# Performance work log

Hardware: AMD Instinct MI355X
Metric: run time of the kernel (lower is better)

Reference implementation:

```python
import jax, jax.numpy as jnp
import numpy as np

B, S, H = 256, 1, 2048
Q_SIZE = 4096        # num_heads * head_dim = 32 * 128
QKV = 4 * H          # expected_linear_qkv = 8192
K_SZ = 4             # conv kernel size
C = 32               # ssm channels
WSCALE = 0.02


def setup_inputs() -> dict:
    key = jax.random.key(0)
    ks = jax.random.split(key, 13)
    return {
        "hidden_states": jax.random.normal(ks[0], (B, S, H), jnp.float32),
        "W_qkv": jax.random.normal(ks[1], (QKV, H), jnp.float32) * WSCALE,
        "b_qkv": jax.random.normal(ks[2], (QKV,), jnp.float32) * WSCALE,
        "W_gate": jax.random.normal(ks[3], (2 * H, H), jnp.float32) * WSCALE,
        "W_alpha": jax.random.normal(ks[4], (C, H), jnp.float32) * WSCALE,
        "W_beta": jax.random.normal(ks[5], (C, H), jnp.float32) * WSCALE,
        "W_out": jax.random.normal(ks[6], (H, 2 * H), jnp.float32) * WSCALE,
        "ssm_state_a": jax.random.normal(ks[7], (C,), jnp.float32),
        "ssm_dt_bias": jax.random.normal(ks[8], (C,), jnp.float32),
        "ssm_norm_weight": jnp.ones((128,), jnp.float32),
        "conv_kernel": jax.random.normal(ks[9], (QKV, K_SZ), jnp.float32) * WSCALE,
        "ssm_state": jax.random.normal(ks[10], (B, C), jnp.float32),
        "conv_state": jax.random.normal(ks[11], (B, K_SZ, QKV), jnp.float32),
    }


def reference(hidden_states, W_qkv, b_qkv, W_gate, W_alpha, W_beta, W_out,
              ssm_state_a, ssm_dt_bias, ssm_norm_weight, conv_kernel,
              ssm_state, conv_state):
    bsz = hidden_states.shape[0]
    # qkv projection (decode: only last token matters downstream)
    qkv = jnp.einsum('bsh,dh->bsd', hidden_states, W_qkv) + b_qkv  # [B,S,4H]
    mixed_qkv = qkv[:, -1, :].astype(jnp.float32)                  # [B,4H]
    hidden_last = hidden_states[:, -1, :]                          # [B,H]

    # roll conv state and append current token, then causal conv1d step
    cs = jnp.concatenate([conv_state[:, 1:, :], mixed_qkv[:, None, :]], axis=1)  # [B,K,4H]
    conv_out = jnp.einsum('bkd,dk->bd', cs, conv_kernel)           # [B,4H]

    target_size = conv_out.shape[-1] - Q_SIZE                      # 2H = 4096
    k_size = target_size // 2                                      # 2048
    core_base = conv_out[:, Q_SIZE:]                               # [B,2H]
    k_proj = core_base[:, :k_size]
    v_proj = core_base[:, k_size:]

    # alpha/beta gating of the SSM state
    a = hidden_last @ W_alpha.T                                    # [B,C]
    b = hidden_last @ W_beta.T                                     # [B,C]
    g = -jnp.exp(ssm_state_a)[None, :] * jax.nn.softplus(a + ssm_dt_bias[None, :])
    beta = jax.nn.sigmoid(b)

    group_width = k_size // C                                      # 64
    v_group = v_proj[:, :group_width * C].reshape(bsz, C, group_width).mean(-1)
    k_group = k_proj[:, :group_width * C].reshape(bsz, C, group_width).mean(-1)

    new_state = jnp.exp(g) * ssm_state + beta * v_group            # [B,C]
    state_signal = new_state * jax.nn.sigmoid(k_group)             # [B,C]

    repeat_factor = target_size // C                               # 128
    expanded = jnp.repeat(state_signal, repeat_factor, axis=-1)[:, :target_size]

    core = core_base + expanded
    core = core * jax.lax.rsqrt(jnp.mean(core * core, axis=-1, keepdims=True) + 1e-6)
    gate = jax.nn.sigmoid(hidden_last @ W_gate.T).astype(jnp.float32)
    core = core * gate * jnp.mean(ssm_norm_weight)
    core = core.astype(hidden_states.dtype)

    out = (core @ W_out.T)[:, None, :]                             # [B,1,H]
    return out
```

## Files before the change

kernel.cpp:

```cpp
#include <hip/hip_runtime.h>
#include <hip/hip_bf16.h>
#include <stdint.h>

#define BSZ 256
#define HDIM 2048
#define NQ 4096
#define N1 8320
#define K1 2048
#define N3 2048
#define K3 4096

typedef __attribute__((ext_vector_type(8))) short bf16x8;
typedef __attribute__((ext_vector_type(4))) float f32x4;

__device__ __forceinline__ unsigned short f2bf(float f) {
  union { float f; unsigned u; } v; v.f = f;
  unsigned r = v.u + 0x7fffu + ((v.u >> 16) & 1u);
  return (unsigned short)(r >> 16);
}

__device__ __forceinline__ void gload_lds16(const void* g, void* lds_uniform) {
  __builtin_amdgcn_global_load_lds(
      (const __attribute__((address_space(1))) unsigned int*)g,
      (__attribute__((address_space(3))) unsigned int*)lds_uniform, 16, 0, 0);
}

__global__ __launch_bounds__(256) void cvt_kernel(const float* __restrict__ x,
                                                  unsigned short* __restrict__ y) {
  int i = (blockIdx.x * 256 + threadIdx.x) * 8;
  float4 a = *(const float4*)(x + i);
  float4 b = *(const float4*)(x + i + 4);
  ushort4 o0 = { f2bf(a.x), f2bf(a.y), f2bf(a.z), f2bf(a.w) };
  ushort4 o1 = { f2bf(b.x), f2bf(b.y), f2bf(b.z), f2bf(b.w) };
  *(ushort4*)(y + i) = o0;
  *(ushort4*)(y + i + 4) = o1;
}

__global__ __launch_bounds__(256) void gemm1_kernel(
    const unsigned short* __restrict__ A16,
    const float* __restrict__ Wqkv, const float* __restrict__ Wgate,
    const float* __restrict__ Walpha, const float* __restrict__ Wbeta,
    float* __restrict__ P) {
  __shared__ unsigned short sA[128 * 32];
  __shared__ unsigned short sB[128 * 32];
  const int tid = threadIdx.x;
  const int lane = tid & 63, wv = tid >> 6;
  const int wr = wv >> 1, wc = wv & 1;
  const int rt = blockIdx.x * 128;
  const int n0 = blockIdx.y * 128;
  const int kbase = blockIdx.z * 1024;

  f32x4 acc[4][4];
#pragma unroll
  for (int i = 0; i < 4; i++)
#pragma unroll
    for (int j = 0; j < 4; j++) { f32x4 z = {0.f, 0.f, 0.f, 0.f}; acc[i][j] = z; }

  for (int ks = 0; ks < 32; ks++) {
    const int k0 = kbase + ks * 32;
#pragma unroll
    for (int it = 0; it < 2; it++) {
      int chunk = (it * 4 + wv) * 1024;
      int f = chunk + lane * 16;
      const char* g = (const char*)A16 + (size_t)(rt + (f >> 6)) * (K1 * 2) + k0 * 2 + (f & 63);
      gload_lds16(g, (char*)sA + chunk);
    }
#pragma unroll
    for (int it = 0; it < 4; it++) {
      int flat = it * 256 + tid;
      int brow = flat >> 3, c4 = flat & 7;
      int n = n0 + brow;
      const float* src;
      if (n < 4096)       src = Wqkv  + (size_t)(4096 + n) * K1;
      else if (n < 8192)  src = Wgate + (size_t)(n - 4096) * K1;
      else if (n < 8224)  src = Walpha + (size_t)(n - 8192) * K1;
      else if (n < 8256)  src = Wbeta + (size_t)(n - 8224) * K1;
      else                src = Walpha;
      float4 v = *(const float4*)(src + k0 + c4 * 4);
      ushort4 o = { f2bf(v.x), f2bf(v.y), f2bf(v.z), f2bf(v.w) };
      *(ushort4*)(sB + brow * 32 + c4 * 4) = o;
    }
    __syncthreads();
    bf16x8 aF[4], bF[4];
#pragma unroll
    for (int i = 0; i < 4; i++)
      aF[i] = *(const bf16x8*)(sA + (wr * 64 + i * 16 + (lane & 15)) * 32 + (lane >> 4) * 8);
#pragma unroll
    for (int j = 0; j < 4; j++)
      bF[j] = *(const bf16x8*)(sB + (wc * 64 + j * 16 + (lane & 15)) * 32 + (lane >> 4) * 8);
#pragma unroll
    for (int i = 0; i < 4; i++)
#pragma unroll
      for (int j = 0; j < 4; j++)
        acc[i][j] = __builtin_amdgcn_mfma_f32_16x16x32_bf16(aF[i], bF[j], acc[i][j], 0, 0, 0);
    __syncthreads();
  }
  float* Pz = P + (size_t)blockIdx.z * (BSZ * (size_t)N1);
#pragma unroll
  for (int i = 0; i < 4; i++) {
    int row = rt + wr * 64 + i * 16 + (lane >> 4) * 4;
#pragma unroll
    for (int j = 0; j < 4; j++) {
      int col = n0 + wc * 64 + j * 16 + (lane & 15);
#pragma unroll
      for (int r = 0; r < 4; r++)
        Pz[(size_t)(row + r) * N1 + col] = acc[i][j][r];
    }
  }
}

__global__ __launch_bounds__(256) void fuse_kernel(
    const float* __restrict__ P,
    const float* __restrict__ bqkv,
    const float* __restrict__ ck,
    const float* __restrict__ cstate,
    const float* __restrict__ ssa,
    const float* __restrict__ dtb,
    const float* __restrict__ nw,
    const float* __restrict__ sstate,
    unsigned short* __restrict__ C16) {
  __shared__ __align__(16) float cb[4096];
  __shared__ float gsum[64];
  __shared__ float ssl[32];
  __shared__ float red[8];
  __shared__ float mw;
  const int b = blockIdx.x, tid = threadIdx.x;
  const float* P0 = P + (size_t)b * N1;
  const float* P1 = P + (size_t)(BSZ + b) * N1;

  if (tid < 64) gsum[tid] = 0.f;
  if (tid == 0) mw = 0.f;
  __syncthreads();
  if (tid < 128) atomicAdd(&mw, nw[tid]);

#pragma unroll
  for (int it = 0; it < 4; it++) {
    int j = (it * 256 + tid) * 4;
    float4 q0 = *(const float4*)(P0 + j);
    float4 q1 = *(const float4*)(P1 + j);
    float4 bq = *(const float4*)(bqkv + NQ + j);
    float mqx = q0.x + q1.x + bq.x, mqy = q0.y + q1.y + bq.y;
    float mqz = q0.z + q1.z + bq.z, mqw = q0.w + q1.w + bq.w;
    const float* csb = cstate + (size_t)b * 4 * 8192 + NQ + j;
    float4 c1 = *(const float4*)(csb + 1 * 8192);
    float4 c2 = *(const float4*)(csb + 2 * 8192);
    float4 c3 = *(const float4*)(csb + 3 * 8192);
    float4 k0v = *(const float4*)(ck + (size_t)(NQ + j) * 4);
    float4 k1v = *(const float4*)(ck + (size_t)(NQ + j + 1) * 4);
    float4 k2v = *(const float4*)(ck + (size_t)(NQ + j + 2) * 4);
    float4 k3v = *(const float4*)(ck + (size_t)(NQ + j + 3) * 4);
    float4 cbv;
    cbv.x = c1.x * k0v.x + c2.x * k0v.y + c3.x * k0v.z + mqx * k0v.w;
    cbv.y = c1.y * k1v.x + c2.y * k1v.y + c3.y * k1v.z + mqy * k1v.w;
    cbv.z = c1.z * k2v.x + c2.z * k2v.y + c3.z * k2v.z + mqz * k2v.w;
    cbv.w = c1.w * k3v.x + c2.w * k3v.y + c3.w * k3v.z + mqw * k3v.w;
    *(float4*)(cb + j) = cbv;
    float s = cbv.x + cbv.y + cbv.z + cbv.w;
    int g = (j < 2048) ? (j >> 6) : (32 + ((j - 2048) >> 6));
    atomicAdd(&gsum[g], s);
  }
  __syncthreads();

  if (tid < 32) {
    float a  = P0[2 * NQ + tid] + P1[2 * NQ + tid];
    float bc = P0[2 * NQ + 32 + tid] + P1[2 * NQ + 32 + tid];
    float kg = gsum[tid] * (1.f / 64.f);
    float vg = gsum[32 + tid] * (1.f / 64.f);
    float x = a + dtb[tid];
    float sp = fmaxf(x, 0.f) + log1pf(expf(-fabsf(x)));
    float g = -expf(ssa[tid]) * sp;
    float beta = 1.f / (1.f + expf(-bc));
    float ns = expf(g) * sstate[b * 32 + tid] + beta * vg;
    ssl[tid] = ns * (1.f / (1.f + expf(-kg)));
  }
  __syncthreads();

  float sq = 0.f;
  float4 c1r[4];
#pragma unroll
  for (int it = 0; it < 4; it++) {
    int j = (it * 256 + tid) * 4;
    float4 v = *(const float4*)(cb + j);
    float sv = ssl[j >> 7];
    v.x += sv; v.y += sv; v.z += sv; v.w += sv;
    c1r[it] = v;
    sq += v.x * v.x + v.y * v.y + v.z * v.z + v.w * v.w;
  }
#pragma unroll
  for (int off = 32; off > 0; off >>= 1) sq += __shfl_down(sq, off, 64);
  if ((tid & 63) == 0) red[tid >> 6] = sq;
  __syncthreads();
  if (tid == 0) {
    float tot = red[0] + red[1] + red[2] + red[3];
    red[4] = rsqrtf(tot * (1.f / 4096.f) + 1e-6f);
    red[5] = mw * (1.f / 128.f);
  }
  __syncthreads();
  float rms = red[4], mwv = red[5];

#pragma unroll
  for (int it = 0; it < 4; it++) {
    int j = (it * 256 + tid) * 4;
    float4 g0 = *(const float4*)(P0 + NQ + j);
    float4 g1 = *(const float4*)(P1 + NQ + j);
    float4 v = c1r[it];
    float ox = v.x * rms * mwv * (1.f / (1.f + expf(-(g0.x + g1.x))));
    float oy = v.y * rms * mwv * (1.f / (1.f + expf(-(g0.y + g1.y))));
    float oz = v.z * rms * mwv * (1.f / (1.f + expf(-(g0.z + g1.z))));
    float ow = v.w * rms * mwv * (1.f / (1.f + expf(-(g0.w + g1.w))));
    ushort4 u = { f2bf(ox), f2bf(oy), f2bf(oz), f2bf(ow) };
    *(ushort4*)(C16 + (size_t)b * 4096 + j) = u;
  }
}

__global__ __launch_bounds__(256) void gemm3_kernel(
    const unsigned short* __restrict__ A16,
    const float* __restrict__ Wout,
    float* __restrict__ out) {
  __shared__ unsigned short sA[128 * 32];
  __shared__ unsigned short sB[128 * 32];
  const int tid = threadIdx.x;
  const int lane = tid & 63, wv = tid >> 6;
  const int wr = wv >> 1, wc = wv & 1;
  const int rt = blockIdx.x * 128;
  const int n0 = blockIdx.y * 128;
  const int kbase = blockIdx.z * 512;

  f32x4 acc[4][4];
#pragma unroll
  for (int i = 0; i < 4; i++)
#pragma unroll
    for (int j = 0; j < 4; j++) { f32x4 z = {0.f, 0.f, 0.f, 0.f}; acc[i][j] = z; }

  for (int ks = 0; ks < 16; ks++) {
    const int k0 = kbase + ks * 32;
#pragma unroll
    for (int it = 0; it < 2; it++) {
      int chunk = (it * 4 + wv) * 1024;
      int f = chunk + lane * 16;
      const char* g = (const char*)A16 + (size_t)(rt + (f >> 6)) * (K3 * 2) + k0 * 2 + (f & 63);
      gload_lds16(g, (char*)sA + chunk);
    }
#pragma unroll
    for (int it = 0; it < 4; it++) {
      int flat = it * 256 + tid;
      int brow = flat >> 3, c4 = flat & 7;
      const float* src = Wout + (size_t)(n0 + brow) * K3;
      float4 v = *(const float4*)(src + k0 + c4 * 4);
      ushort4 o = { f2bf(v.x), f2bf(v.y), f2bf(v.z), f2bf(v.w) };
      *(ushort4*)(sB + brow * 32 + c4 * 4) = o;
    }
    __syncthreads();
    bf16x8 aF[4], bF[4];
#pragma unroll
    for (int i = 0; i < 4; i++)
      aF[i] = *(const bf16x8*)(sA + (wr * 64 + i * 16 + (lane & 15)) * 32 + (lane >> 4) * 8);
#pragma unroll
    for (int j = 0; j < 4; j++)
      bF[j] = *(const bf16x8*)(sB + (wc * 64 + j * 16 + (lane & 15)) * 32 + (lane >> 4) * 8);
#pragma unroll
    for (int i = 0; i < 4; i++)
#pragma unroll
      for (int j = 0; j < 4; j++)
        acc[i][j] = __builtin_amdgcn_mfma_f32_16x16x32_bf16(aF[i], bF[j], acc[i][j], 0, 0, 0);
    __syncthreads();
  }
#pragma unroll
  for (int i = 0; i < 4; i++) {
    int row = rt + wr * 64 + i * 16 + (lane >> 4) * 4;
#pragma unroll
    for (int j = 0; j < 4; j++) {
      int col = n0 + wc * 64 + j * 16 + (lane & 15);
#pragma unroll
      for (int r = 0; r < 4; r++)
        atomicAdd(&out[(size_t)(row + r) * N3 + col], acc[i][j][r]);
    }
  }
}

extern "C" void kernel_launch(void* const* d_in, const int* in_sizes, int n_in,
                              void* d_out, int out_size, void* d_ws, size_t ws_size,
                              hipStream_t stream) {
  const float* hidden = (const float*)d_in[0];
  const float* Wqkv   = (const float*)d_in[1];
  const float* bqkv   = (const float*)d_in[2];
  const float* Wgate  = (const float*)d_in[3];
  const float* Walpha = (const float*)d_in[4];
  const float* Wbeta  = (const float*)d_in[5];
  const float* Wout   = (const float*)d_in[6];
  const float* ssa    = (const float*)d_in[7];
  const float* dtb    = (const float*)d_in[8];
  const float* nw     = (const float*)d_in[9];
  const float* ck     = (const float*)d_in[10];
  const float* sstate = (const float*)d_in[11];
  const float* cstate = (const float*)d_in[12];
  float* out = (float*)d_out;

  char* ws = (char*)d_ws;
  unsigned short* A16 = (unsigned short*)ws;
  float* P = (float*)(ws + (1 << 20));
  unsigned short* C16 = (unsigned short*)(ws + (1 << 20) + (size_t)2 * BSZ * N1 * 4);

  hipMemsetAsync(d_out, 0, (size_t)BSZ * N3 * sizeof(float), stream);
  cvt_kernel<<<256, 256, 0, stream>>>(hidden, A16);
  gemm1_kernel<<<dim3(2, 65, 2), 256, 0, stream>>>(A16, Wqkv, Wgate, Walpha, Wbeta, P);
  fuse_kernel<<<256, 256, 0, stream>>>(P, bqkv, ck, cstate, ssa, dtb, nw, sstate, C16);
  gemm3_kernel<<<dim3(2, 16, 8), 256, 0, stream>>>(C16, Wout, out);
}
```

Baseline: 249.8 us.

## Double-buffer GEMM tiles, halve N-tile, atomic split-K reduction, widen fuse kernel

```diff
diff --git a/kernel.cpp b/kernel.cpp
--- a/kernel.cpp
+++ b/kernel.cpp
@@ -3,7 +3,6 @@
 #include <stdint.h>
 
 #define BSZ 256
-#define HDIM 2048
 #define NQ 4096
 #define N1 8320
 #define K1 2048
@@ -17,6 +16,13 @@
   union { float f; unsigned u; } v; v.f = f;
   unsigned r = v.u + 0x7fffu + ((v.u >> 16) & 1u);
   return (unsigned short)(r >> 16);
+}
+
+__device__ __forceinline__ bf16x8 pack8(float4 a, float4 b) {
+  union { bf16x8 v; unsigned short u[8]; } o;
+  o.u[0] = f2bf(a.x); o.u[1] = f2bf(a.y); o.u[2] = f2bf(a.z); o.u[3] = f2bf(a.w);
+  o.u[4] = f2bf(b.x); o.u[5] = f2bf(b.y); o.u[6] = f2bf(b.z); o.u[7] = f2bf(b.w);
+  return o.v;
 }
 
 __device__ __forceinline__ void gload_lds16(const void* g, void* lds_uniform) {
@@ -41,75 +47,81 @@
     const float* __restrict__ Wqkv, const float* __restrict__ Wgate,
     const float* __restrict__ Walpha, const float* __restrict__ Wbeta,
     float* __restrict__ P) {
-  __shared__ unsigned short sA[128 * 32];
-  __shared__ unsigned short sB[128 * 32];
-  const int tid = threadIdx.x;
-  const int lane = tid & 63, wv = tid >> 6;
+  __shared__ unsigned short sA[2][128 * 32];
+  __shared__ unsigned short sB[2][64 * 32];
+  const int tid = threadIdx.x, lane = tid & 63, wv = tid >> 6;
   const int wr = wv >> 1, wc = wv & 1;
   const int rt = blockIdx.x * 128;
-  const int n0 = blockIdx.y * 128;
-  const int kbase = blockIdx.z * 1024;
-
-  f32x4 acc[4][4];
+  const int n0 = blockIdx.y * 64;
+  const int kb = blockIdx.z * 1024;
+
+  const int brow = tid >> 2, bcol = (tid & 3) * 8;
+  const float* bsrc;
+  {
+    int n = n0 + brow;
+    const float* s;
+    if (n < 4096)       s = Wqkv  + (size_t)(4096 + n) * K1;
+    else if (n < 8192)  s = Wgate + (size_t)(n - 4096) * K1;
+    else if (n < 8224)  s = Walpha + (size_t)(n - 8192) * K1;
+    else if (n < 8256)  s = Wbeta + (size_t)(n - 8224) * K1;
+    else                s = Walpha;
+    bsrc = s + kb + bcol;
+  }
+  const char* asrc0 = (const char*)(A16 + (size_t)(rt + (tid >> 2)) * K1 + kb) + (tid & 3) * 16;
+  const char* asrc1 = asrc0 + (size_t)64 * K1 * 2;
+
+  f32x4 acc[4][2];
 #pragma unroll
   for (int i = 0; i < 4; i++)
 #pragma unroll
-    for (int j = 0; j < 4; j++) { f32x4 z = {0.f, 0.f, 0.f, 0.f}; acc[i][j] = z; }
+    for (int j = 0; j < 2; j++) { f32x4 z = {0.f, 0.f, 0.f, 0.f}; acc[i][j] = z; }
+
+  float4 pb0, pb1;
+  gload_lds16(asrc0, (char*)sA[0] + wv * 1024);
+  gload_lds16(asrc1, (char*)sA[0] + 4096 + wv * 1024);
+  pb0 = *(const float4*)bsrc;
+  pb1 = *(const float4*)(bsrc + 4);
+  *(bf16x8*)&sB[0][brow * 32 + bcol] = pack8(pb0, pb1);
 
   for (int ks = 0; ks < 32; ks++) {
-    const int k0 = kbase + ks * 32;
-#pragma unroll
-    for (int it = 0; it < 2; it++) {
-      int chunk = (it * 4 + wv) * 1024;
-      int f = chunk + lane * 16;
-      const char* g = (const char*)A16 + (size_t)(rt + (f >> 6)) * (K1 * 2) + k0 * 2 + (f & 63);
-      gload_lds16(g, (char*)sA + chunk);
+    const int cur = ks & 1, nxt = cur ^ 1;
+    __syncthreads();
+    if (ks + 1 < 32) {
+      gload_lds16(asrc0 + (ks + 1) * 64, (char*)sA[nxt] + wv * 1024);
+      gload_lds16(asrc1 + (ks + 1) * 64, (char*)sA[nxt] + 4096 + wv * 1024);
+      pb0 = *(const float4*)(bsrc + (ks + 1) * 32);
+      pb1 = *(const float4*)(bsrc + (ks + 1) * 32 + 4);
     }
-#pragma unroll
-    for (int it = 0; it < 4; it++) {
-      int flat = it * 256 + tid;
-      int brow = flat >> 3, c4 = flat & 7;
-      int n = n0 + brow;
-      const float* src;
-      if (n < 4096)       src = Wqkv  + (size_t)(4096 + n) * K1;
-      else if (n < 8192)  src = Wgate + (size_t)(n - 4096) * K1;
-      else if (n < 8224)  src = Walpha + (size_t)(n - 8192) * K1;
-      else if (n < 8256)  src = Wbeta + (size_t)(n - 8224) * K1;
-      else                src = Walpha;
-      float4 v = *(const float4*)(src + k0 + c4 * 4);
-      ushort4 o = { f2bf(v.x), f2bf(v.y), f2bf(v.z), f2bf(v.w) };
-      *(ushort4*)(sB + brow * 32 + c4 * 4) = o;
-    }
-    __syncthreads();
-    bf16x8 aF[4], bF[4];
+    bf16x8 aF[4], bF[2];
 #pragma unroll
     for (int i = 0; i < 4; i++)
-      aF[i] = *(const bf16x8*)(sA + (wr * 64 + i * 16 + (lane & 15)) * 32 + (lane >> 4) * 8);
-#pragma unroll
-    for (int j = 0; j < 4; j++)
-      bF[j] = *(const bf16x8*)(sB + (wc * 64 + j * 16 + (lane & 15)) * 32 + (lane >> 4) * 8);
+      aF[i] = *(const bf16x8*)(&sA[cur][(wr * 64 + i * 16 + (lane & 15)) * 32 + (lane >> 4) * 8]);
+#pragma unroll
+    for (int j = 0; j < 2; j++)
+      bF[j] = *(const bf16x8*)(&sB[cur][(wc * 32 + j * 16 + (lane & 15)) * 32 + (lane >> 4) * 8]);
 #pragma unroll
     for (int i = 0; i < 4; i++)
 #pragma unroll
-      for (int j = 0; j < 4; j++)
+      for (int j = 0; j < 2; j++)
         acc[i][j] = __builtin_amdgcn_mfma_f32_16x16x32_bf16(aF[i], bF[j], acc[i][j], 0, 0, 0);
-    __syncthreads();
-  }
-  float* Pz = P + (size_t)blockIdx.z * (BSZ * (size_t)N1);
+    if (ks + 1 < 32)
+      *(bf16x8*)&sB[nxt][brow * 32 + bcol] = pack8(pb0, pb1);
+  }
+
 #pragma unroll
   for (int i = 0; i < 4; i++) {
     int row = rt + wr * 64 + i * 16 + (lane >> 4) * 4;
 #pragma unroll
-    for (int j = 0; j < 4; j++) {
-      int col = n0 + wc * 64 + j * 16 + (lane & 15);
+    for (int j = 0; j < 2; j++) {
+      int col = n0 + wc * 32 + j * 16 + (lane & 15);
 #pragma unroll
       for (int r = 0; r < 4; r++)
-        Pz[(size_t)(row + r) * N1 + col] = acc[i][j][r];
+        atomicAdd(&P[(size_t)(row + r) * N1 + col], acc[i][j][r]);
     }
   }
 }
 
-__global__ __launch_bounds__(256) void fuse_kernel(
+__global__ __launch_bounds__(512) void fuse_kernel(
     const float* __restrict__ P,
     const float* __restrict__ bqkv,
     const float* __restrict__ ck,
@@ -122,29 +134,28 @@
   __shared__ __align__(16) float cb[4096];
   __shared__ float gsum[64];
   __shared__ float ssl[32];
-  __shared__ float red[8];
-  __shared__ float mw;
+  __shared__ float red[16];
   const int b = blockIdx.x, tid = threadIdx.x;
-  const float* P0 = P + (size_t)b * N1;
-  const float* P1 = P + (size_t)(BSZ + b) * N1;
-
-  if (tid < 64) gsum[tid] = 0.f;
-  if (tid == 0) mw = 0.f;
-  __syncthreads();
-  if (tid < 128) atomicAdd(&mw, nw[tid]);
-
-#pragma unroll
-  for (int it = 0; it < 4; it++) {
-    int j = (it * 256 + tid) * 4;
-    float4 q0 = *(const float4*)(P0 + j);
-    float4 q1 = *(const float4*)(P1 + j);
+  const int lane = tid & 63, wv = tid >> 6;
+  const float* Pb = P + (size_t)b * N1;
+
+  if (wv == 0) {
+    float m = nw[lane] + nw[lane + 64];
+#pragma unroll
+    for (int off = 32; off; off >>= 1) m += __shfl_down(m, off, 64);
+    if (lane == 0) red[8] = m * (1.f / 128.f);
+  }
+
+#pragma unroll
+  for (int it = 0; it < 2; it++) {
+    int j = (it * 512 + tid) * 4;
+    float4 q  = *(const float4*)(Pb + j);
     float4 bq = *(const float4*)(bqkv + NQ + j);
-    float mqx = q0.x + q1.x + bq.x, mqy = q0.y + q1.y + bq.y;
-    float mqz = q0.z + q1.z + bq.z, mqw = q0.w + q1.w + bq.w;
+    float mqx = q.x + bq.x, mqy = q.y + bq.y, mqz = q.z + bq.z, mqw = q.w + bq.w;
     const float* csb = cstate + (size_t)b * 4 * 8192 + NQ + j;
-    float4 c1 = *(const float4*)(csb + 1 * 8192);
-    float4 c2 = *(const float4*)(csb + 2 * 8192);
-    float4 c3 = *(const float4*)(csb + 3 * 8192);
+    float4 c1 = *(const float4*)(csb + 8192);
+    float4 c2 = *(const float4*)(csb + 16384);
+    float4 c3 = *(const float4*)(csb + 24576);
     float4 k0v = *(const float4*)(ck + (size_t)(NQ + j) * 4);
     float4 k1v = *(const float4*)(ck + (size_t)(NQ + j + 1) * 4);
     float4 k2v = *(const float4*)(ck + (size_t)(NQ + j + 2) * 4);
@@ -156,14 +167,15 @@
     cbv.w = c1.w * k3v.x + c2.w * k3v.y + c3.w * k3v.z + mqw * k3v.w;
     *(float4*)(cb + j) = cbv;
     float s = cbv.x + cbv.y + cbv.z + cbv.w;
-    int g = (j < 2048) ? (j >> 6) : (32 + ((j - 2048) >> 6));
-    atomicAdd(&gsum[g], s);
+    s += __shfl_xor(s, 1, 64); s += __shfl_xor(s, 2, 64);
+    s += __shfl_xor(s, 4, 64); s += __shfl_xor(s, 8, 64);
+    if ((lane & 15) == 0) gsum[(it * 512 + tid) >> 4] = s;
   }
   __syncthreads();
 
   if (tid < 32) {
-    float a  = P0[2 * NQ + tid] + P1[2 * NQ + tid];
-    float bc = P0[2 * NQ + 32 + tid] + P1[2 * NQ + 32 + tid];
+    float a  = Pb[8192 + tid];
+    float bc = Pb[8224 + tid];
     float kg = gsum[tid] * (1.f / 64.f);
     float vg = gsum[32 + tid] * (1.f / 64.f);
     float x = a + dtb[tid];
@@ -171,15 +183,15 @@
     float g = -expf(ssa[tid]) * sp;
     float beta = 1.f / (1.f + expf(-bc));
     float ns = expf(g) * sstate[b * 32 + tid] + beta * vg;
-    ssl[tid] = ns * (1.f / (1.f + expf(-kg)));
+    ssl[tid] = ns / (1.f + expf(-kg));
   }
   __syncthreads();
 
   float sq = 0.f;
-  float4 c1r[4];
-#pragma unroll
-  for (int it = 0; it < 4; it++) {
-    int j = (it * 256 + tid) * 4;
+  float4 c1r[2];
+#pragma unroll
+  for (int it = 0; it < 2; it++) {
+    int j = (it * 512 + tid) * 4;
     float4 v = *(const float4*)(cb + j);
     float sv = ssl[j >> 7];
     v.x += sv; v.y += sv; v.z += sv; v.w += sv;
@@ -187,27 +199,25 @@
     sq += v.x * v.x + v.y * v.y + v.z * v.z + v.w * v.w;
   }
 #pragma unroll
-  for (int off = 32; off > 0; off >>= 1) sq += __shfl_down(sq, off, 64);
-  if ((tid & 63) == 0) red[tid >> 6] = sq;
+  for (int off = 32; off; off >>= 1) sq += __shfl_down(sq, off, 64);
+  if (lane == 0) red[wv] = sq;
   __syncthreads();
   if (tid == 0) {
-    float tot = red[0] + red[1] + red[2] + red[3];
-    red[4] = rsqrtf(tot * (1.f / 4096.f) + 1e-6f);
-    red[5] = mw * (1.f / 128.f);
+    float t = red[0] + red[1] + red[2] + red[3] + red[4] + red[5] + red[6] + red[7];
+    red[9] = rsqrtf(t * (1.f / 4096.f) + 1e-6f);
   }
   __syncthreads();
-  float rms = red[4], mwv = red[5];
-
-#pragma unroll
-  for (int it = 0; it < 4; it++) {
-    int j = (it * 256 + tid) * 4;
-    float4 g0 = *(const float4*)(P0 + NQ + j);
-    float4 g1 = *(const float4*)(P1 + NQ + j);
+  float rms = red[9], mwv = red[8];
+
+#pragma unroll
+  for (int it = 0; it < 2; it++) {
+    int j = (it * 512 + tid) * 4;
+    float4 g0 = *(const float4*)(Pb + NQ + j);
     float4 v = c1r[it];
-    float ox = v.x * rms * mwv * (1.f / (1.f + expf(-(g0.x + g1.x))));
-    float oy = v.y * rms * mwv * (1.f / (1.f + expf(-(g0.y + g1.y))));
-    float oz = v.z * rms * mwv * (1.f / (1.f + expf(-(g0.z + g1.z))));
-    float ow = v.w * rms * mwv * (1.f / (1.f + expf(-(g0.w + g1.w))));
+    float ox = v.x * rms * mwv / (1.f + expf(-g0.x));
+    float oy = v.y * rms * mwv / (1.f + expf(-g0.y));
+    float oz = v.z * rms * mwv / (1.f + expf(-g0.z));
+    float ow = v.w * rms * mwv / (1.f + expf(-g0.w));
     ushort4 u = { f2bf(ox), f2bf(oy), f2bf(oz), f2bf(ow) };
     *(ushort4*)(C16 + (size_t)b * 4096 + j) = u;
   }
@@ -217,60 +227,63 @@
     const unsigned short* __restrict__ A16,
     const float* __restrict__ Wout,
     float* __restrict__ out) {
-  __shared__ unsigned short sA[128 * 32];
-  __shared__ unsigned short sB[128 * 32];
-  const int tid = threadIdx.x;
-  const int lane = tid & 63, wv = tid >> 6;
+  __shared__ unsigned short sA[2][128 * 32];
+  __shared__ unsigned short sB[2][64 * 32];
+  const int tid = threadIdx.x, lane = tid & 63, wv = tid >> 6;
   const int wr = wv >> 1, wc = wv & 1;
   const int rt = blockIdx.x * 128;
-  const int n0 = blockIdx.y * 128;
-  const int kbase = blockIdx.z * 512;
-
-  f32x4 acc[4][4];
+  const int n0 = blockIdx.y * 64;
+  const int kb = blockIdx.z * 512;
+
+  const int brow = tid >> 2, bcol = (tid & 3) * 8;
+  const float* bsrc = Wout + (size_t)(n0 + brow) * K3 + kb + bcol;
+  const char* asrc0 = (const char*)(A16 + (size_t)(rt + (tid >> 2)) * K3 + kb) + (tid & 3) * 16;
+  const char* asrc1 = asrc0 + (size_t)64 * K3 * 2;
+
+  f32x4 acc[4][2];
 #pragma unroll
   for (int i = 0; i < 4; i++)
 #pragma unroll
-    for (int j = 0; j < 4; j++) { f32x4 z = {0.f, 0.f, 0.f, 0.f}; acc[i][j] = z; }
+    for (int j = 0; j < 2; j++) { f32x4 z = {0.f, 0.f, 0.f, 0.f}; acc[i][j] = z; }
+
+  float4 pb0, pb1;
+  gload_lds16(asrc0, (char*)sA[0] + wv * 1024);
+  gload_lds16(asrc1, (char*)sA[0] + 4096 + wv * 1024);
+  pb0 = *(const float4*)bsrc;
+  pb1 = *(const float4*)(bsrc + 4);
+  *(bf16x8*)&sB[0][brow * 32 + bcol] = pack8(pb0, pb1);
 
   for (int ks = 0; ks < 16; ks++) {
-    const int k0 = kbase + ks * 32;
-#pragma unroll
-    for (int it = 0; it < 2; it++) {
-      int chunk = (it * 4 + wv) * 1024;
-      int f = chunk + lane * 16;
-      const char* g = (const char*)A16 + (size_t)(rt + (f >> 6)) * (K3 * 2) + k0 * 2 + (f & 63);
-      gload_lds16(g, (char*)sA + chunk);
+    const int cur = ks & 1, nxt = cur ^ 1;
+    __syncthreads();
+    if (ks + 1 < 16) {
+      gload_lds16(asrc0 + (ks + 1) * 64, (char*)sA[nxt] + wv * 1024);
+      gload_lds16(asrc1 + (ks + 1) * 64, (char*)sA[nxt] + 4096 + wv * 1024);
+      pb0 = *(const float4*)(bsrc + (ks + 1) * 32);
+      pb1 = *(const float4*)(bsrc + (ks + 1) * 32 + 4);
     }
-#pragma unroll
-    for (int it = 0; it < 4; it++) {
-      int flat = it * 256 + tid;
-      int brow = flat >> 3, c4 = flat & 7;
-      const float* src = Wout + (size_t)(n0 + brow) * K3;
-      float4 v = *(const float4*)(src + k0 + c4 * 4);
-      ushort4 o = { f2bf(v.x), f2bf(v.y), f2bf(v.z), f2bf(v.w) };
-      *(ushort4*)(sB + brow * 32 + c4 * 4) = o;
-    }
-    __syncthreads();
-    bf16x8 aF[4], bF[4];
+    bf16x8 aF[4], bF[2];
 #pragma unroll
     for (int i = 0; i < 4; i++)
-      aF[i] = *(const bf16x8*)(sA + (wr * 64 + i * 16 + (lane & 15)) * 32 + (lane >> 4) * 8);
-#pragma unroll
-    for (int j = 0; j < 4; j++)
-      bF[j] = *(const bf16x8*)(sB + (wc * 64 + j * 16 + (lane & 15)) * 32 + (lane >> 4) * 8);
+      aF[i] = *(const bf16x8*)(&sA[cur][(wr * 64 + i * 16 + (lane & 15)) * 32 + (lane >> 4) * 8]);
+#pragma unroll
+    for (int j = 0; j < 2; j++)
+      bF[j] = *(const bf16x8*)(&sB[cur][(wc * 32 + j * 16 + (lane & 15)) * 32 + (lane >> 4) * 8]);
 #pragma unroll
     for (int i = 0; i < 4; i++)
 #pragma unroll
-      for (int j = 0; j < 4; j++)
+      for (int j = 0; j < 2; j++)
         acc[i][j] = __builtin_amdgcn_mfma_f32_16x16x32_bf16(aF[i], bF[j], acc[i][j], 0, 0, 0);
-    __syncthreads();
-  }
+    if (ks + 1 < 16)
+      *(bf16x8*)&sB[nxt][brow * 32 + bcol] = pack8(pb0, pb1);
+  }
+
 #pragma unroll
   for (int i = 0; i < 4; i++) {
     int row = rt + wr * 64 + i * 16 + (lane >> 4) * 4;
 #pragma unroll
-    for (int j = 0; j < 4; j++) {
-      int col = n0 + wc * 64 + j * 16 + (lane & 15);
+    for (int j = 0; j < 2; j++) {
+      int col = n0 + wc * 32 + j * 16 + (lane & 15);
 #pragma unroll
       for (int r = 0; r < 4; r++)
         atomicAdd(&out[(size_t)(row + r) * N3 + col], acc[i][j][r]);
@@ -299,11 +312,12 @@
   char* ws = (char*)d_ws;
   unsigned short* A16 = (unsigned short*)ws;
   float* P = (float*)(ws + (1 << 20));
-  unsigned short* C16 = (unsigned short*)(ws + (1 << 20) + (size_t)2 * BSZ * N1 * 4);
+  unsigned short* C16 = (unsigned short*)(ws + (1 << 20) + 8519680);
 
   hipMemsetAsync(d_out, 0, (size_t)BSZ * N3 * sizeof(float), stream);
+  hipMemsetAsync(P, 0, (size_t)BSZ * N1 * sizeof(float), stream);
   cvt_kernel<<<256, 256, 0, stream>>>(hidden, A16);
-  gemm1_kernel<<<dim3(2, 65, 2), 256, 0, stream>>>(A16, Wqkv, Wgate, Walpha, Wbeta, P);
-  fuse_kernel<<<256, 256, 0, stream>>>(P, bqkv, ck, cstate, ssa, dtb, nw, sstate, C16);
-  gemm3_kernel<<<dim3(2, 16, 8), 256, 0, stream>>>(C16, Wout, out);
-}
+  gemm1_kernel<<<dim3(2, 130, 2), 256, 0, stream>>>(A16, Wqkv, Wgate, Walpha, Wbeta, P);
+  fuse_kernel<<<256, 512, 0, stream>>>(P, bqkv, ck, cstate, ssa, dtb, nw, sstate, C16);
+  gemm3_kernel<<<dim3(2, 32, 8), 256, 0, stream>>>(C16, Wout, out);
+}
```

Result: no change. 248.2 us (-0.6%).
